# Optimization experiments

Hardware: AMD Instinct MI355X
Metric: run time of the kernel (lower is better)

The kernel has to match this reference:

```python
import jax, jax.numpy as jnp
import numpy as np

D_MODEL = 1024
D_INTERNAL = 64
SEQ = 2048
BATCH = 4


def setup_inputs() -> dict:
    key = jax.random.key(0)
    ks = jax.random.split(key, 9)
    s = 1.0 / np.sqrt(D_MODEL)
    return {
        "query": jax.random.normal(ks[0], (SEQ, BATCH, D_MODEL), jnp.float32),
        "key": jax.random.normal(ks[1], (SEQ, BATCH, D_MODEL), jnp.float32),
        "value": jax.random.normal(ks[2], (SEQ, BATCH, D_MODEL), jnp.float32),
        "Wq": jax.random.normal(ks[3], (D_MODEL, D_INTERNAL), jnp.float32) * s,
        "bq": jnp.zeros((D_INTERNAL,), jnp.float32),
        "Wk": jax.random.normal(ks[4], (D_MODEL, D_INTERNAL), jnp.float32) * s,
        "bk": jnp.zeros((D_INTERNAL,), jnp.float32),
        "Wv": jax.random.normal(ks[5], (D_MODEL, D_MODEL), jnp.float32) * s,
        "bv": jnp.zeros((D_MODEL,), jnp.float32),
    }


def reference(query, key, value, Wq, bq, Wk, bk, Wv, bv):
    # inputs: (S, B, D); project then move batch first -> (B, S, *)
    q = (query @ Wq + bq).transpose(1, 0, 2)          # (B, S, d_int)
    k = (key @ Wk + bk).transpose(1, 0, 2)            # (B, S, d_int)
    v = (value @ Wv + bv).transpose(1, 0, 2)          # (B, S, D)
    scores = jnp.einsum("bqd,bkd->bqk", q, k) / jnp.sqrt(jnp.float32(D_INTERNAL))
    probs = jax.nn.softmax(scores, axis=-1)           # row softmax over keys
    # extra renormalization over the QUERY axis (dim=1), as in the source
    probs = probs / (1e-9 + probs.sum(axis=1, keepdims=True))
    aten = jnp.einsum("bqk,bkd->bqd", probs, v).transpose(1, 0, 2)  # (S, B, D)
    return aten, probs
```

## Files before the change

### kernel.cpp

```cpp
#include <hip/hip_runtime.h>
#include <math.h>

#define SEQ 2048
#define BATCH 4
#define DM 1024
#define DI 64

typedef __attribute__((ext_vector_type(8))) short bf16x8;
typedef __attribute__((ext_vector_type(4))) float f32x4;

__device__ __forceinline__ unsigned short f2bf(float f) {
  unsigned u = __float_as_uint(f);
  unsigned r = (u + 0x7fff + ((u >> 16) & 1)) >> 16;
  return (unsigned short)r;
}

__device__ __forceinline__ float bf2f(unsigned short u) {
  return __uint_as_float((unsigned)u << 16);
}

__device__ __forceinline__ void gload_lds16(const void* g, void* l) {
  __builtin_amdgcn_global_load_lds(
      (const __attribute__((address_space(1))) unsigned int*)g,
      (__attribute__((address_space(3))) unsigned int*)l, 16, 0, 0);
}


__global__ __launch_bounds__(256) void trans_kernel(
    const float* __restrict__ Wq, const float* __restrict__ Wk,
    const float* __restrict__ Wv,
    unsigned short* __restrict__ WqkT, unsigned short* __restrict__ WvT,
    float* __restrict__ colsum) {
  __shared__ unsigned short t[64][65];
  int lx = threadIdx.x & 63, ly = threadIdx.x >> 6;
  if (blockIdx.y < 16) {
    int bx = blockIdx.x * 64, by = blockIdx.y * 64;
#pragma unroll
    for (int i = 0; i < 64; i += 4)
      t[ly + i][lx] = f2bf(Wv[(size_t)(bx + ly + i) * DM + by + lx]);
    __syncthreads();
#pragma unroll
    for (int i = 0; i < 64; i += 4)
      WvT[(size_t)(by + ly + i) * DM + bx + lx] = t[lx][ly + i];
  } else if (blockIdx.y < 18) {
    int which = blockIdx.y - 16;
    const float* W = which ? Wk : Wq;
    unsigned short* WT = WqkT + (size_t)which * DI * DM;
    int bx = blockIdx.x * 64;
#pragma unroll
    for (int i = 0; i < 64; i += 4)
      t[ly + i][lx] = f2bf(W[(size_t)(bx + ly + i) * DI + lx]);
    __syncthreads();
#pragma unroll
    for (int i = 0; i < 64; i += 4)
      WT[(size_t)(ly + i) * DM + bx + lx] = t[lx][ly + i];
  } else {
    int idx = blockIdx.x * 256 + threadIdx.x;
    colsum[idx] = 0.f;
    colsum[idx + 4096] = 0.f;
  }
}

__global__ __launch_bounds__(256) void qkproj_mfma(
    const float* __restrict__ query, const float* __restrict__ key,
    const unsigned short* __restrict__ WqkT,
    const float* __restrict__ bq, const float* __restrict__ bk,
    unsigned short* __restrict__ qbf, unsigned short* __restrict__ kbf) {
  __shared__ __align__(16) unsigned short As[32 * 32];
  __shared__ __align__(16) unsigned short Bs[64 * 32];
  int which = blockIdx.y;
  const float* A = (which ? key : query) + (size_t)blockIdx.x * 32 * DM;
  const unsigned short* Bt = WqkT + (size_t)which * DI * DM;
  const float* bias = which ? bk : bq;
  unsigned short* outp = which ? kbf : qbf;

  const int tid = threadIdx.x;
  const int lane = tid & 63, wave = tid >> 6;
  const int lrow = lane & 15, quad = lane >> 4;
  const int wr = (wave >> 1) * 16;
  const int wc = (wave & 1) * 32;
  const int sw = (quad ^ ((lrow >> 1) & 3)) * 8;
  f32x4 acc[2] = {};

  const int am = tid >> 3, asub = tid & 7;
  const int akc = asub * 4;
  const int asl = am * 32 + (((asub >> 1) ^ ((am >> 1) & 3)) * 8) + (asub & 1) * 4;
  const int bn = tid >> 2;
  const int bkc = (((tid & 3) ^ ((bn >> 1) & 3)) * 8);

  for (int k0 = 0; k0 < DM; k0 += 32) {
    __syncthreads();
    gload_lds16(Bt + (size_t)bn * DM + k0 + bkc, Bs + wave * 512);
    float4 a = *(const float4*)(A + (size_t)am * DM + k0 + akc);
    ushort4 h;
    h.x = f2bf(a.x); h.y = f2bf(a.y); h.z = f2bf(a.z); h.w = f2bf(a.w);
    *(ushort4*)&As[asl] = h;
    __syncthreads();
    bf16x8 af = *(const bf16x8*)&As[(wr + lrow) * 32 + sw];
    bf16x8 b0 = *(const bf16x8*)&Bs[(wc + lrow) * 32 + sw];
    bf16x8 b1 = *(const bf16x8*)&Bs[(wc + 16 + lrow) * 32 + sw];
    acc[0] = __builtin_amdgcn_mfma_f32_16x16x32_bf16(af, b0, acc[0], 0, 0, 0);
    acc[1] = __builtin_amdgcn_mfma_f32_16x16x32_bf16(af, b1, acc[1], 0, 0, 0);
  }
  int sbase = blockIdx.x * 8 + (wr >> 2) + quad;
#pragma unroll
  for (int ni = 0; ni < 2; ++ni) {
    int n = wc + ni * 16 + lrow;
    float bb = bias[n];
#pragma unroll
    for (int reg = 0; reg < 4; ++reg)
      outp[((size_t)reg * SEQ + sbase) * DI + n] = f2bf(acc[ni][reg] + bb);
  }
}

__global__ __launch_bounds__(256) void vcast_kernel(
    const float* __restrict__ value, unsigned short* __restrict__ vbf) {
  size_t i = ((size_t)blockIdx.x * 256 + threadIdx.x) * 8;
  float4 a = *(const float4*)(value + i);
  float4 b = *(const float4*)(value + i + 4);
  bf16x8 h;
  h[0] = (short)f2bf(a.x); h[1] = (short)f2bf(a.y);
  h[2] = (short)f2bf(a.z); h[3] = (short)f2bf(a.w);
  h[4] = (short)f2bf(b.x); h[5] = (short)f2bf(b.y);
  h[6] = (short)f2bf(b.z); h[7] = (short)f2bf(b.w);
  *(bf16x8*)(vbf + i) = h;
}

__device__ __forceinline__ void mfma_core_bb_12864(
    const unsigned short* __restrict__ At, int lda,
    const unsigned short* __restrict__ Bt, int ldb,
    int K, f32x4 (&acc)[4][2],
    unsigned short* As, unsigned short* Bs) {
  const int tid  = threadIdx.x;
  const int lane = tid & 63;
  const int wave = tid >> 6;
  const int wr   = (wave >> 1) * 64;
  const int wc   = (wave & 1) * 32;
  const int lrow = lane & 15;
  const int quad = lane >> 4;
  const int sw   = (quad ^ ((lrow >> 1) & 3)) * 8;
  const int bn   = tid >> 2;
  const int bkc  = ((tid & 3) ^ ((bn >> 1) & 3)) * 8;

  for (int k0 = 0; k0 < K; k0 += 32) {
    __syncthreads();
#pragma unroll
    for (int it = 0; it < 2; ++it) {
      int c = it * 256 + tid;
      int m = c >> 2, kc = ((c & 3) ^ ((m >> 1) & 3)) * 8;
      gload_lds16(At + (size_t)m * lda + k0 + kc,
                  As + (size_t)(it * 256 + wave * 64) * 8);
    }
    gload_lds16(Bt + (size_t)bn * ldb + k0 + bkc, Bs + wave * 512);
    __syncthreads();
    bf16x8 af[4], bfr[2];
#pragma unroll
    for (int mi = 0; mi < 4; ++mi)
      af[mi] = *(const bf16x8*)&As[(wr + mi * 16 + lrow) * 32 + sw];
#pragma unroll
    for (int ni = 0; ni < 2; ++ni)
      bfr[ni] = *(const bf16x8*)&Bs[(wc + ni * 16 + lrow) * 32 + sw];
#pragma unroll
    for (int mi = 0; mi < 4; ++mi)
#pragma unroll
      for (int ni = 0; ni < 2; ++ni)
        acc[mi][ni] = __builtin_amdgcn_mfma_f32_16x16x32_bf16(
            af[mi], bfr[ni], acc[mi][ni], 0, 0, 0);
  }
}

__global__ __launch_bounds__(256) void vproj_mfma(
    const unsigned short* __restrict__ vbf, const unsigned short* __restrict__ WvT,
    const float* __restrict__ bv, const float* __restrict__ invcol,
    unsigned short* __restrict__ vT) {
  __shared__ __align__(16) unsigned short As[128 * 32];
  __shared__ __align__(16) unsigned short Bs[64 * 32];
  __shared__ __align__(16) unsigned short ep[64 * 4 * 32];
  __shared__ float icl[128];
  f32x4 acc[4][2] = {};
  int m0 = blockIdx.x * 128, n0 = blockIdx.y * 64;
  int s0 = m0 >> 2;
  if (threadIdx.x < 128)
    icl[threadIdx.x] = invcol[(size_t)(threadIdx.x >> 5) * SEQ + s0 + (threadIdx.x & 31)];
  mfma_core_bb_12864(vbf + (size_t)m0 * DM, DM, WvT + (size_t)n0 * DM, DM, DM,
                     acc, As, Bs);
  const int tid = threadIdx.x;
  const int lane = tid & 63, wave = tid >> 6;
  const int wr = (wave >> 1) * 64, wc = (wave & 1) * 32;
  const int lrow = lane & 15, quad = lane >> 4;
#pragma unroll
  for (int mi = 0; mi < 4; ++mi) {
    int ss = (wr >> 2) + mi * 4 + quad;
#pragma unroll
    for (int ni = 0; ni < 2; ++ni) {
      int nn = wc + ni * 16 + lrow;
      float bias = bv[n0 + nn];
      int swz = (nn & 3) << 3;
#pragma unroll
      for (int reg = 0; reg < 4; ++reg)
        ep[nn * 128 + reg * 32 + (ss ^ swz)] =
            f2bf((acc[mi][ni][reg] + bias) * icl[reg * 32 + ss]);
    }
  }
  __syncthreads();
#pragma unroll
  for (int t8 = 0; t8 < 4; ++t8) {
    int c = t8 * 256 + tid;
    int ss8 = (c & 3) * 8, b = (c >> 2) & 3, nn = c >> 4;
    uint4 vv = *(const uint4*)&ep[nn * 128 + b * 32 + (ss8 ^ ((nn & 3) << 3))];
    *(uint4*)&vT[((size_t)(b * DM + n0 + nn)) * SEQ + s0 + ss8] = vv;
  }
}

__global__ __launch_bounds__(256) void scores_rowpanel(
    const unsigned short* __restrict__ qbf, const unsigned short* __restrict__ kbf,
    unsigned short* __restrict__ ebf, float* __restrict__ invrs,
    float* __restrict__ colsum) {
  __shared__ __align__(16) unsigned short Qs[16 * 64];
  __shared__ __align__(16) unsigned short Ks[128 * 64];
  __shared__ float red[4][16];
  __shared__ float irl[16];
  int bid = blockIdx.x;
  int x = bid & 7, j = bid >> 3;
  int b = x >> 1;
  int q0 = (j * 2 + (x & 1)) * 16;

  const int tid = threadIdx.x;
  const int lane = tid & 63, wave = tid >> 6;
  const int lrow = lane & 15, quad = lane >> 4;
  const int wc = wave * 32;
  const int sw = (quad ^ ((lrow >> 1) & 3)) * 8;
  const unsigned short* Q = qbf + ((size_t)b * SEQ + q0) * DI;
  const unsigned short* Kp = kbf + (size_t)b * SEQ * DI;
  unsigned short* C = ebf + (size_t)b * SEQ * SEQ;

  if (tid < 128) {
    int m = tid >> 3, kk = (tid >> 2) & 1, jj = tid & 3;
    gload_lds16(Q + (size_t)m * DI + kk * 32 + ((jj ^ ((m >> 1) & 3)) * 8),
                Qs + (size_t)(tid & ~63) * 8);
  }

  float rsum[4] = {0.f, 0.f, 0.f, 0.f};
  for (int kt = 0; kt < 16; ++kt) {
    int k0 = kt * 128;
    __syncthreads();
#pragma unroll
    for (int it = 0; it < 4; ++it) {
      int c = it * 256 + tid;
      int n = c >> 3, kk = (c >> 2) & 1, jj = c & 3;
      gload_lds16(Kp + (size_t)(k0 + n) * DI + kk * 32 + ((jj ^ ((n >> 1) & 3)) * 8),
                  Ks + (size_t)(it * 256 + wave * 64) * 8);
    }
    __syncthreads();
    bf16x8 af[2], bfr[2][2];
#pragma unroll
    for (int kk = 0; kk < 2; ++kk) {
      af[kk] = *(const bf16x8*)&Qs[lrow * 64 + kk * 32 + sw];
#pragma unroll
      for (int ni = 0; ni < 2; ++ni)
        bfr[ni][kk] = *(const bf16x8*)&Ks[(wc + ni * 16 + lrow) * 64 + kk * 32 + sw];
    }
    f32x4 acc[2] = {};
#pragma unroll
    for (int ni = 0; ni < 2; ++ni) {
      acc[ni] = __builtin_amdgcn_mfma_f32_16x16x32_bf16(af[0], bfr[ni][0], acc[ni], 0, 0, 0);
      acc[ni] = __builtin_amdgcn_mfma_f32_16x16x32_bf16(af[1], bfr[ni][1], acc[ni], 0, 0, 0);
    }
#pragma unroll
    for (int ni = 0; ni < 2; ++ni) {
      int n = k0 + wc + ni * 16 + lrow;
#pragma unroll
      for (int reg = 0; reg < 4; ++reg) {
        float e = __expf(acc[ni][reg] * 0.125f);
        C[(size_t)(q0 + quad * 4 + reg) * SEQ + n] = f2bf(e);
        rsum[reg] += e;
      }
    }
  }
  __threadfence_block();
#pragma unroll
  for (int reg = 0; reg < 4; ++reg) {
    rsum[reg] += __shfl_xor(rsum[reg], 1);
    rsum[reg] += __shfl_xor(rsum[reg], 2);
    rsum[reg] += __shfl_xor(rsum[reg], 4);
    rsum[reg] += __shfl_xor(rsum[reg], 8);
  }
  if (lrow == 0) {
#pragma unroll
    for (int reg = 0; reg < 4; ++reg) red[wave][quad * 4 + reg] = rsum[reg];
  }
  __syncthreads();
  if (tid < 16) {
    float t = red[0][tid] + red[1][tid] + red[2][tid] + red[3][tid];
    float inv = 1.0f / t;
    invrs[(size_t)b * SEQ + q0 + tid] = inv;
    irl[tid] = inv;
  }
  __syncthreads();
  int k8 = tid * 8;
  float cs[8] = {0.f, 0.f, 0.f, 0.f, 0.f, 0.f, 0.f, 0.f};
#pragma unroll 4
  for (int i = 0; i < 16; ++i) {
    const unsigned short* row = C + (size_t)(q0 + i) * SEQ + k8;
    ushort4 h0 = *(const ushort4*)(row);
    ushort4 h1 = *(const ushort4*)(row + 4);
    float ir = irl[i];
    cs[0] += bf2f(h0.x) * ir; cs[1] += bf2f(h0.y) * ir;
    cs[2] += bf2f(h0.z) * ir; cs[3] += bf2f(h0.w) * ir;
    cs[4] += bf2f(h1.x) * ir; cs[5] += bf2f(h1.y) * ir;
    cs[6] += bf2f(h1.z) * ir; cs[7] += bf2f(h1.w) * ir;
  }
#pragma unroll
  for (int jj = 0; jj < 8; ++jj)
    atomicAdd(&colsum[b * SEQ + k8 + jj], cs[jj]);
}

__global__ void recip_kernel(const float* __restrict__ in,
                             float* __restrict__ outp, float eps, int n) {
  int i = blockIdx.x * blockDim.x + threadIdx.x;
  if (i < n) outp[i] = 1.0f / (eps + in[i]);
}

__global__ __launch_bounds__(256) void probsout_kernel(
    const unsigned short* __restrict__ ebf, const float* __restrict__ invrs,
    const float* __restrict__ invcol, float* __restrict__ probs) {
  size_t f = ((size_t)blockIdx.x * 256 + threadIdx.x) * 4;
  int b = (int)(f >> 22);
  int q = (int)((f >> 11) & 2047);
  int k = (int)(f & 2047);
  ushort4 h = *(const ushort4*)(ebf + f);
  float ir = invrs[b * SEQ + q];
  float4 c = *(const float4*)(invcol + b * SEQ + k);
  float4 p;
  p.x = bf2f(h.x) * ir * c.x;
  p.y = bf2f(h.y) * ir * c.y;
  p.z = bf2f(h.z) * ir * c.z;
  p.w = bf2f(h.w) * ir * c.w;
  *(float4*)(probs + f) = p;
}

__global__ __launch_bounds__(256) void aten_mfma(
    const unsigned short* __restrict__ ebf, const unsigned short* __restrict__ vT,
    const float* __restrict__ invrs, float* __restrict__ out) {
  __shared__ __align__(16) unsigned short As[128 * 64];
  __shared__ __align__(16) unsigned short Bs[128 * 64];
  __shared__ float irs[128];
  int bid = blockIdx.x;
  int wg = (bid & 7) * 64 + (bid >> 3);
  int mb = wg & 15, nb = (wg >> 4) & 7, b = wg >> 7;
  int m0 = mb * 128, n0 = nb * 128;
  if (threadIdx.x < 128)
    irs[threadIdx.x] = invrs[(size_t)b * SEQ + m0 + threadIdx.x];
  const unsigned short* At = ebf + ((size_t)b * SEQ + m0) * SEQ;
  const unsigned short* Bt = vT + ((size_t)b * DM + n0) * SEQ;

  const int tid = threadIdx.x;
  const int lane = tid & 63, wave = tid >> 6;
  const int wr = (wave >> 1) * 64, wc = (wave & 1) * 64;
  const int lrow = lane & 15, quad = lane >> 4;
  const int sw = (quad ^ ((lrow >> 1) & 3)) * 8;

  f32x4 acc[4][4] = {};
  for (int k0 = 0; k0 < SEQ; k0 += 64) {
    __syncthreads();
#pragma unroll
    for (int it = 0; it < 4; ++it) {
      int c = it * 256 + tid;
      int m = c >> 3, kk = (c >> 2) & 1, jj = c & 3;
      gload_lds16(At + (size_t)m * SEQ + k0 + kk * 32 + ((jj ^ ((m >> 1) & 3)) * 8),
                  As + (size_t)(it * 256 + wave * 64) * 8);
    }
#pragma unroll
    for (int it = 0; it < 4; ++it) {
      int c = it * 256 + tid;
      int n = c >> 3, kk = (c >> 2) & 1, jj = c & 3;
      gload_lds16(Bt + (size_t)n * SEQ + k0 + kk * 32 + ((jj ^ ((n >> 1) & 3)) * 8),
                  Bs + (size_t)(it * 256 + wave * 64) * 8);
    }
    __syncthreads();
    bf16x8 bfr[4][2];
#pragma unroll
    for (int ni = 0; ni < 4; ++ni)
#pragma unroll
      for (int kk = 0; kk < 2; ++kk)
        bfr[ni][kk] = *(const bf16x8*)&Bs[(wc + ni * 16 + lrow) * 64 + kk * 32 + sw];
#pragma unroll
    for (int mi = 0; mi < 4; ++mi) {
      bf16x8 a0 = *(const bf16x8*)&As[(wr + mi * 16 + lrow) * 64 + sw];
      bf16x8 a1 = *(const bf16x8*)&As[(wr + mi * 16 + lrow) * 64 + 32 + sw];
#pragma unroll
      for (int ni = 0; ni < 4; ++ni) {
        acc[mi][ni] = __builtin_amdgcn_mfma_f32_16x16x32_bf16(a0, bfr[ni][0], acc[mi][ni], 0, 0, 0);
        acc[mi][ni] = __builtin_amdgcn_mfma_f32_16x16x32_bf16(a1, bfr[ni][1], acc[mi][ni], 0, 0, 0);
      }
    }
  }
#pragma unroll
  for (int mi = 0; mi < 4; ++mi) {
    int rb = wr + mi * 16 + quad * 4;
    int qr = m0 + rb;
#pragma unroll
    for (int ni = 0; ni < 4; ++ni) {
      int n = n0 + wc + ni * 16 + lrow;
#pragma unroll
      for (int reg = 0; reg < 4; ++reg)
        out[(size_t)(qr + reg) * (BATCH * DM) + b * DM + n] =
            acc[mi][ni][reg] * irs[rb + reg];
    }
  }
}

extern "C" void kernel_launch(void* const* d_in, const int* in_sizes, int n_in,
                              void* d_out, int out_size, void* d_ws, size_t ws_size,
                              hipStream_t stream) {
  const float* query = (const float*)d_in[0];
  const float* key   = (const float*)d_in[1];
  const float* value = (const float*)d_in[2];
  const float* Wq    = (const float*)d_in[3];
  const float* bq    = (const float*)d_in[4];
  const float* Wk    = (const float*)d_in[5];
  const float* bk    = (const float*)d_in[6];
  const float* Wv    = (const float*)d_in[7];
  const float* bv    = (const float*)d_in[8];

  float* out   = (float*)d_out;
  float* probs = out + (size_t)SEQ * BATCH * DM;

  unsigned short* WvT  = (unsigned short*)d_ws;
  unsigned short* WqkT = WvT  + (size_t)DM * DM;
  unsigned short* qbf  = WqkT + (size_t)2 * DI * DM;
  unsigned short* kbf  = qbf  + (size_t)BATCH * SEQ * DI;
  unsigned short* vT   = kbf  + (size_t)BATCH * SEQ * DI;
  unsigned short* ebf  = vT   + (size_t)BATCH * DM * SEQ;
  unsigned short* vbf  = ebf  + (size_t)BATCH * SEQ * SEQ;
  float* colsum = (float*)(vbf + (size_t)BATCH * SEQ * DM);
  float* invrs  = colsum + (size_t)BATCH * SEQ;
  float* invcol = invrs  + (size_t)BATCH * SEQ;

  trans_kernel<<<dim3(16, 19), 256, 0, stream>>>(Wq, Wk, Wv, WqkT, WvT, colsum);
  qkproj_mfma<<<dim3(SEQ * BATCH / 32, 2), 256, 0, stream>>>(
      query, key, WqkT, bq, bk, qbf, kbf);
  vcast_kernel<<<(SEQ * BATCH * DM / 8) / 256, 256, 0, stream>>>(value, vbf);
  scores_rowpanel<<<dim3(512), 256, 0, stream>>>(qbf, kbf, ebf, invrs, colsum);
  recip_kernel<<<(BATCH * SEQ + 255) / 256, 256, 0, stream>>>(
      colsum, invcol, 1e-9f, BATCH * SEQ);
  vproj_mfma<<<dim3(SEQ * BATCH / 128, DM / 64), 256, 0, stream>>>(
      vbf, WvT, bv, invcol, vT);
  aten_mfma<<<dim3(512), 256, 0, stream>>>(ebf, vT, invrs, out);
  probsout_kernel<<<(BATCH * SEQ * SEQ / 4) / 256, 256, 0, stream>>>(
      ebf, invrs, invcol, probs);
}
```

Measured before the change: 334.2 us.

## Merge independent kernels into shared launches and inline column reciprocal

New measurement: 378.5 us. 1.13x slower.

```diff
diff --git a/kernel.cpp b/kernel.cpp
--- a/kernel.cpp
+++ b/kernel.cpp
@@ -61,20 +61,34 @@
   }
 }
 
-__global__ __launch_bounds__(256) void qkproj_mfma(
+__global__ __launch_bounds__(256) void qkv_mix(
     const float* __restrict__ query, const float* __restrict__ key,
     const unsigned short* __restrict__ WqkT,
     const float* __restrict__ bq, const float* __restrict__ bk,
-    unsigned short* __restrict__ qbf, unsigned short* __restrict__ kbf) {
+    unsigned short* __restrict__ qbf, unsigned short* __restrict__ kbf,
+    const float* __restrict__ value, unsigned short* __restrict__ vbf) {
   __shared__ __align__(16) unsigned short As[32 * 32];
   __shared__ __align__(16) unsigned short Bs[64 * 32];
-  int which = blockIdx.y;
-  const float* A = (which ? key : query) + (size_t)blockIdx.x * 32 * DM;
+  int id = blockIdx.x;
+  const int tid = threadIdx.x;
+  if (id >= 512) {
+    size_t i = ((size_t)(id - 512) * 256 + tid) * 8;
+    float4 a = *(const float4*)(value + i);
+    float4 b = *(const float4*)(value + i + 4);
+    bf16x8 h;
+    h[0] = (short)f2bf(a.x); h[1] = (short)f2bf(a.y);
+    h[2] = (short)f2bf(a.z); h[3] = (short)f2bf(a.w);
+    h[4] = (short)f2bf(b.x); h[5] = (short)f2bf(b.y);
+    h[6] = (short)f2bf(b.z); h[7] = (short)f2bf(b.w);
+    *(bf16x8*)(vbf + i) = h;
+    return;
+  }
+  int bx = id & 255, which = id >> 8;
+  const float* A = (which ? key : query) + (size_t)bx * 32 * DM;
   const unsigned short* Bt = WqkT + (size_t)which * DI * DM;
   const float* bias = which ? bk : bq;
   unsigned short* outp = which ? kbf : qbf;
 
-  const int tid = threadIdx.x;
   const int lane = tid & 63, wave = tid >> 6;
   const int lrow = lane & 15, quad = lane >> 4;
   const int wr = (wave >> 1) * 16;
@@ -102,7 +116,7 @@
     acc[0] = __builtin_amdgcn_mfma_f32_16x16x32_bf16(af, b0, acc[0], 0, 0, 0);
     acc[1] = __builtin_amdgcn_mfma_f32_16x16x32_bf16(af, b1, acc[1], 0, 0, 0);
   }
-  int sbase = blockIdx.x * 8 + (wr >> 2) + quad;
+  int sbase = bx * 8 + (wr >> 2) + quad;
 #pragma unroll
   for (int ni = 0; ni < 2; ++ni) {
     int n = wc + ni * 16 + lrow;
@@ -111,19 +125,6 @@
     for (int reg = 0; reg < 4; ++reg)
       outp[((size_t)reg * SEQ + sbase) * DI + n] = f2bf(acc[ni][reg] + bb);
   }
-}
-
-__global__ __launch_bounds__(256) void vcast_kernel(
-    const float* __restrict__ value, unsigned short* __restrict__ vbf) {
-  size_t i = ((size_t)blockIdx.x * 256 + threadIdx.x) * 8;
-  float4 a = *(const float4*)(value + i);
-  float4 b = *(const float4*)(value + i + 4);
-  bf16x8 h;
-  h[0] = (short)f2bf(a.x); h[1] = (short)f2bf(a.y);
-  h[2] = (short)f2bf(a.z); h[3] = (short)f2bf(a.w);
-  h[4] = (short)f2bf(b.x); h[5] = (short)f2bf(b.y);
-  h[6] = (short)f2bf(b.z); h[7] = (short)f2bf(b.w);
-  *(bf16x8*)(vbf + i) = h;
 }
 
 __device__ __forceinline__ void mfma_core_bb_12864(
@@ -171,7 +172,7 @@
 
 __global__ __launch_bounds__(256) void vproj_mfma(
     const unsigned short* __restrict__ vbf, const unsigned short* __restrict__ WvT,
-    const float* __restrict__ bv, const float* __restrict__ invcol,
+    const float* __restrict__ bv, const float* __restrict__ colsum,
     unsigned short* __restrict__ vT) {
   __shared__ __align__(16) unsigned short As[128 * 32];
   __shared__ __align__(16) unsigned short Bs[64 * 32];
@@ -181,7 +182,8 @@
   int m0 = blockIdx.x * 128, n0 = blockIdx.y * 64;
   int s0 = m0 >> 2;
   if (threadIdx.x < 128)
-    icl[threadIdx.x] = invcol[(size_t)(threadIdx.x >> 5) * SEQ + s0 + (threadIdx.x & 31)];
+    icl[threadIdx.x] =
+        1.0f / (1e-9f + colsum[(size_t)(threadIdx.x >> 5) * SEQ + s0 + (threadIdx.x & 31)]);
   mfma_core_bb_12864(vbf + (size_t)m0 * DM, DM, WvT + (size_t)n0 * DM, DM, DM,
                      acc, As, Bs);
   const int tid = threadIdx.x;
@@ -315,46 +317,43 @@
     atomicAdd(&colsum[b * SEQ + k8 + jj], cs[jj]);
 }
 
-__global__ void recip_kernel(const float* __restrict__ in,
-                             float* __restrict__ outp, float eps, int n) {
-  int i = blockIdx.x * blockDim.x + threadIdx.x;
-  if (i < n) outp[i] = 1.0f / (eps + in[i]);
-}
-
-__global__ __launch_bounds__(256) void probsout_kernel(
-    const unsigned short* __restrict__ ebf, const float* __restrict__ invrs,
-    const float* __restrict__ invcol, float* __restrict__ probs) {
-  size_t f = ((size_t)blockIdx.x * 256 + threadIdx.x) * 4;
-  int b = (int)(f >> 22);
-  int q = (int)((f >> 11) & 2047);
-  int k = (int)(f & 2047);
-  ushort4 h = *(const ushort4*)(ebf + f);
-  float ir = invrs[b * SEQ + q];
-  float4 c = *(const float4*)(invcol + b * SEQ + k);
-  float4 p;
-  p.x = bf2f(h.x) * ir * c.x;
-  p.y = bf2f(h.y) * ir * c.y;
-  p.z = bf2f(h.z) * ir * c.z;
-  p.w = bf2f(h.w) * ir * c.w;
-  *(float4*)(probs + f) = p;
-}
-
-__global__ __launch_bounds__(256) void aten_mfma(
+__global__ __launch_bounds__(256) void aten_probs(
     const unsigned short* __restrict__ ebf, const unsigned short* __restrict__ vT,
-    const float* __restrict__ invrs, float* __restrict__ out) {
+    const float* __restrict__ invrs, const float* __restrict__ colsum,
+    float* __restrict__ out, float* __restrict__ probs) {
   __shared__ __align__(16) unsigned short As[128 * 64];
   __shared__ __align__(16) unsigned short Bs[128 * 64];
   __shared__ float irs[128];
-  int bid = blockIdx.x;
-  int wg = (bid & 7) * 64 + (bid >> 3);
+  int id = blockIdx.x;
+  const int tid = threadIdx.x;
+  if (id >= 512) {
+    size_t base = ((size_t)(id - 512) * 4096 + tid);
+#pragma unroll 4
+    for (int t = 0; t < 16; ++t) {
+      size_t f = (base + (size_t)t * 256) * 4;
+      int b = (int)(f >> 22);
+      int q = (int)((f >> 11) & 2047);
+      int k = (int)(f & 2047);
+      ushort4 h = *(const ushort4*)(ebf + f);
+      float ir = invrs[b * SEQ + q];
+      float4 c = *(const float4*)(colsum + b * SEQ + k);
+      float4 p;
+      p.x = bf2f(h.x) * ir * (1.0f / (1e-9f + c.x));
+      p.y = bf2f(h.y) * ir * (1.0f / (1e-9f + c.y));
+      p.z = bf2f(h.z) * ir * (1.0f / (1e-9f + c.z));
+      p.w = bf2f(h.w) * ir * (1.0f / (1e-9f + c.w));
+      *(float4*)(probs + f) = p;
+    }
+    return;
+  }
+  int wg = (id & 7) * 64 + (id >> 3);
   int mb = wg & 15, nb = (wg >> 4) & 7, b = wg >> 7;
   int m0 = mb * 128, n0 = nb * 128;
-  if (threadIdx.x < 128)
-    irs[threadIdx.x] = invrs[(size_t)b * SEQ + m0 + threadIdx.x];
+  if (tid < 128)
+    irs[tid] = invrs[(size_t)b * SEQ + m0 + tid];
   const unsigned short* At = ebf + ((size_t)b * SEQ + m0) * SEQ;
   const unsigned short* Bt = vT + ((size_t)b * DM + n0) * SEQ;
 
-  const int tid = threadIdx.x;
   const int lane = tid & 63, wave = tid >> 6;
   const int wr = (wave >> 1) * 64, wc = (wave & 1) * 64;
   const int lrow = lane & 15, quad = lane >> 4;
@@ -435,18 +434,13 @@
   unsigned short* vbf  = ebf  + (size_t)BATCH * SEQ * SEQ;
   float* colsum = (float*)(vbf + (size_t)BATCH * SEQ * DM);
   float* invrs  = colsum + (size_t)BATCH * SEQ;
-  float* invcol = invrs  + (size_t)BATCH * SEQ;
 
   trans_kernel<<<dim3(16, 19), 256, 0, stream>>>(Wq, Wk, Wv, WqkT, WvT, colsum);
-  qkproj_mfma<<<dim3(SEQ * BATCH / 32, 2), 256, 0, stream>>>(
-      query, key, WqkT, bq, bk, qbf, kbf);
-  vcast_kernel<<<(SEQ * BATCH * DM / 8) / 256, 256, 0, stream>>>(value, vbf);
+  qkv_mix<<<dim3(512 + SEQ * BATCH * DM / 8 / 256), 256, 0, stream>>>(
+      query, key, WqkT, bq, bk, qbf, kbf, value, vbf);
   scores_rowpanel<<<dim3(512), 256, 0, stream>>>(qbf, kbf, ebf, invrs, colsum);
-  recip_kernel<<<(BATCH * SEQ + 255) / 256, 256, 0, stream>>>(
-      colsum, invcol, 1e-9f, BATCH * SEQ);
   vproj_mfma<<<dim3(SEQ * BATCH / 128, DM / 64), 256, 0, stream>>>(
-      vbf, WvT, bv, invcol, vT);
-  aten_mfma<<<dim3(512), 256, 0, stream>>>(ebf, vT, invrs, out);
-  probsout_kernel<<<(BATCH * SEQ * SEQ / 4) / 256, 256, 0, stream>>>(
-      ebf, invrs, invcol, probs);
-}
+      vbf, WvT, bv, colsum, vT);
+  aten_probs<<<dim3(512 + 1024), 256, 0, stream>>>(
+      ebf, vT, invrs, colsum, out, probs);
+}
```

## Split column-sum into its own kernel, fold reciprocal into consumers, change LDS swizzle

Applied to the files above, without the earlier changes.

Result: faster. 316.8 us (-5.2%).

```diff
diff --git a/kernel.cpp b/kernel.cpp
--- a/kernel.cpp
+++ b/kernel.cpp
@@ -171,7 +171,7 @@
 
 __global__ __launch_bounds__(256) void vproj_mfma(
     const unsigned short* __restrict__ vbf, const unsigned short* __restrict__ WvT,
-    const float* __restrict__ bv, const float* __restrict__ invcol,
+    const float* __restrict__ bv, const float* __restrict__ colsum,
     unsigned short* __restrict__ vT) {
   __shared__ __align__(16) unsigned short As[128 * 32];
   __shared__ __align__(16) unsigned short Bs[64 * 32];
@@ -181,7 +181,8 @@
   int m0 = blockIdx.x * 128, n0 = blockIdx.y * 64;
   int s0 = m0 >> 2;
   if (threadIdx.x < 128)
-    icl[threadIdx.x] = invcol[(size_t)(threadIdx.x >> 5) * SEQ + s0 + (threadIdx.x & 31)];
+    icl[threadIdx.x] =
+        1.0f / (1e-9f + colsum[(size_t)(threadIdx.x >> 5) * SEQ + s0 + (threadIdx.x & 31)]);
   mfma_core_bb_12864(vbf + (size_t)m0 * DM, DM, WvT + (size_t)n0 * DM, DM, DM,
                      acc, As, Bs);
   const int tid = threadIdx.x;
@@ -214,12 +215,10 @@
 
 __global__ __launch_bounds__(256) void scores_rowpanel(
     const unsigned short* __restrict__ qbf, const unsigned short* __restrict__ kbf,
-    unsigned short* __restrict__ ebf, float* __restrict__ invrs,
-    float* __restrict__ colsum) {
+    unsigned short* __restrict__ ebf, float* __restrict__ invrs) {
   __shared__ __align__(16) unsigned short Qs[16 * 64];
   __shared__ __align__(16) unsigned short Ks[128 * 64];
   __shared__ float red[4][16];
-  __shared__ float irl[16];
   int bid = blockIdx.x;
   int x = bid & 7, j = bid >> 3;
   int b = x >> 1;
@@ -229,14 +228,16 @@
   const int lane = tid & 63, wave = tid >> 6;
   const int lrow = lane & 15, quad = lane >> 4;
   const int wc = wave * 32;
-  const int sw = (quad ^ ((lrow >> 1) & 3)) * 8;
+  const int r7 = lrow & 7;
+  const int c0 = (quad ^ r7) * 8;
+  const int c1 = ((quad + 4) ^ r7) * 8;
   const unsigned short* Q = qbf + ((size_t)b * SEQ + q0) * DI;
   const unsigned short* Kp = kbf + (size_t)b * SEQ * DI;
   unsigned short* C = ebf + (size_t)b * SEQ * SEQ;
 
   if (tid < 128) {
-    int m = tid >> 3, kk = (tid >> 2) & 1, jj = tid & 3;
-    gload_lds16(Q + (size_t)m * DI + kk * 32 + ((jj ^ ((m >> 1) & 3)) * 8),
+    int m = tid >> 3, pos = tid & 7;
+    gload_lds16(Q + (size_t)m * DI + ((pos ^ (m & 7)) * 8),
                 Qs + (size_t)(tid & ~63) * 8);
   }
 
@@ -247,18 +248,19 @@
 #pragma unroll
     for (int it = 0; it < 4; ++it) {
       int c = it * 256 + tid;
-      int n = c >> 3, kk = (c >> 2) & 1, jj = c & 3;
-      gload_lds16(Kp + (size_t)(k0 + n) * DI + kk * 32 + ((jj ^ ((n >> 1) & 3)) * 8),
+      int n = c >> 3, pos = c & 7;
+      gload_lds16(Kp + (size_t)(k0 + n) * DI + ((pos ^ (n & 7)) * 8),
                   Ks + (size_t)(it * 256 + wave * 64) * 8);
     }
     __syncthreads();
     bf16x8 af[2], bfr[2][2];
-#pragma unroll
-    for (int kk = 0; kk < 2; ++kk) {
-      af[kk] = *(const bf16x8*)&Qs[lrow * 64 + kk * 32 + sw];
-#pragma unroll
-      for (int ni = 0; ni < 2; ++ni)
-        bfr[ni][kk] = *(const bf16x8*)&Ks[(wc + ni * 16 + lrow) * 64 + kk * 32 + sw];
+    af[0] = *(const bf16x8*)&Qs[lrow * 64 + c0];
+    af[1] = *(const bf16x8*)&Qs[lrow * 64 + c1];
+#pragma unroll
+    for (int ni = 0; ni < 2; ++ni) {
+      int rr = (wc + ni * 16 + lrow) * 64;
+      bfr[ni][0] = *(const bf16x8*)&Ks[rr + c0];
+      bfr[ni][1] = *(const bf16x8*)&Ks[rr + c1];
     }
     f32x4 acc[2] = {};
 #pragma unroll
@@ -277,7 +279,6 @@
       }
     }
   }
-  __threadfence_block();
 #pragma unroll
   for (int reg = 0; reg < 4; ++reg) {
     rsum[reg] += __shfl_xor(rsum[reg], 1);
@@ -292,50 +293,39 @@
   __syncthreads();
   if (tid < 16) {
     float t = red[0][tid] + red[1][tid] + red[2][tid] + red[3][tid];
-    float inv = 1.0f / t;
-    invrs[(size_t)b * SEQ + q0 + tid] = inv;
-    irl[tid] = inv;
-  }
-  __syncthreads();
-  int k8 = tid * 8;
-  float cs[8] = {0.f, 0.f, 0.f, 0.f, 0.f, 0.f, 0.f, 0.f};
+    invrs[(size_t)b * SEQ + q0 + tid] = 1.0f / t;
+  }
+}
+
+__global__ __launch_bounds__(256) void colsum_kernel(
+    const unsigned short* __restrict__ ebf, const float* __restrict__ invrs,
+    float* __restrict__ colsum) {
+  int b = blockIdx.z;
+  int k = blockIdx.x * 256 + threadIdx.x;
+  int q0 = blockIdx.y * 128;
+  const unsigned short* p = ebf + (size_t)b * SEQ * SEQ + (size_t)q0 * SEQ + k;
+  const float* ir = invrs + (size_t)b * SEQ + q0;
+  float sum = 0.f;
 #pragma unroll 4
-  for (int i = 0; i < 16; ++i) {
-    const unsigned short* row = C + (size_t)(q0 + i) * SEQ + k8;
-    ushort4 h0 = *(const ushort4*)(row);
-    ushort4 h1 = *(const ushort4*)(row + 4);
-    float ir = irl[i];
-    cs[0] += bf2f(h0.x) * ir; cs[1] += bf2f(h0.y) * ir;
-    cs[2] += bf2f(h0.z) * ir; cs[3] += bf2f(h0.w) * ir;
-    cs[4] += bf2f(h1.x) * ir; cs[5] += bf2f(h1.y) * ir;
-    cs[6] += bf2f(h1.z) * ir; cs[7] += bf2f(h1.w) * ir;
-  }
-#pragma unroll
-  for (int jj = 0; jj < 8; ++jj)
-    atomicAdd(&colsum[b * SEQ + k8 + jj], cs[jj]);
-}
-
-__global__ void recip_kernel(const float* __restrict__ in,
-                             float* __restrict__ outp, float eps, int n) {
-  int i = blockIdx.x * blockDim.x + threadIdx.x;
-  if (i < n) outp[i] = 1.0f / (eps + in[i]);
+  for (int i = 0; i < 128; ++i) sum += bf2f(p[(size_t)i * SEQ]) * ir[i];
+  atomicAdd(&colsum[b * SEQ + k], sum);
 }
 
 __global__ __launch_bounds__(256) void probsout_kernel(
     const unsigned short* __restrict__ ebf, const float* __restrict__ invrs,
-    const float* __restrict__ invcol, float* __restrict__ probs) {
+    const float* __restrict__ colsum, float* __restrict__ probs) {
   size_t f = ((size_t)blockIdx.x * 256 + threadIdx.x) * 4;
   int b = (int)(f >> 22);
   int q = (int)((f >> 11) & 2047);
   int k = (int)(f & 2047);
   ushort4 h = *(const ushort4*)(ebf + f);
   float ir = invrs[b * SEQ + q];
-  float4 c = *(const float4*)(invcol + b * SEQ + k);
+  float4 c = *(const float4*)(colsum + b * SEQ + k);
   float4 p;
-  p.x = bf2f(h.x) * ir * c.x;
-  p.y = bf2f(h.y) * ir * c.y;
-  p.z = bf2f(h.z) * ir * c.z;
-  p.w = bf2f(h.w) * ir * c.w;
+  p.x = bf2f(h.x) * ir * (1.0f / (1e-9f + c.x));
+  p.y = bf2f(h.y) * ir * (1.0f / (1e-9f + c.y));
+  p.z = bf2f(h.z) * ir * (1.0f / (1e-9f + c.z));
+  p.w = bf2f(h.w) * ir * (1.0f / (1e-9f + c.w));
   *(float4*)(probs + f) = p;
 }
 
@@ -358,7 +348,9 @@
   const int lane = tid & 63, wave = tid >> 6;
   const int wr = (wave >> 1) * 64, wc = (wave & 1) * 64;
   const int lrow = lane & 15, quad = lane >> 4;
-  const int sw = (quad ^ ((lrow >> 1) & 3)) * 8;
+  const int r7 = lrow & 7;
+  const int c0 = (quad ^ r7) * 8;
+  const int c1 = ((quad + 4) ^ r7) * 8;
 
   f32x4 acc[4][4] = {};
   for (int k0 = 0; k0 < SEQ; k0 += 64) {
@@ -366,28 +358,30 @@
 #pragma unroll
     for (int it = 0; it < 4; ++it) {
       int c = it * 256 + tid;
-      int m = c >> 3, kk = (c >> 2) & 1, jj = c & 3;
-      gload_lds16(At + (size_t)m * SEQ + k0 + kk * 32 + ((jj ^ ((m >> 1) & 3)) * 8),
+      int m = c >> 3, pos = c & 7;
+      gload_lds16(At + (size_t)m * SEQ + k0 + ((pos ^ (m & 7)) * 8),
                   As + (size_t)(it * 256 + wave * 64) * 8);
     }
 #pragma unroll
     for (int it = 0; it < 4; ++it) {
       int c = it * 256 + tid;
-      int n = c >> 3, kk = (c >> 2) & 1, jj = c & 3;
-      gload_lds16(Bt + (size_t)n * SEQ + k0 + kk * 32 + ((jj ^ ((n >> 1) & 3)) * 8),
+      int n = c >> 3, pos = c & 7;
+      gload_lds16(Bt + (size_t)n * SEQ + k0 + ((pos ^ (n & 7)) * 8),
                   Bs + (size_t)(it * 256 + wave * 64) * 8);
     }
     __syncthreads();
     bf16x8 bfr[4][2];
 #pragma unroll
-    for (int ni = 0; ni < 4; ++ni)
-#pragma unroll
-      for (int kk = 0; kk < 2; ++kk)
-        bfr[ni][kk] = *(const bf16x8*)&Bs[(wc + ni * 16 + lrow) * 64 + kk * 32 + sw];
+    for (int ni = 0; ni < 4; ++ni) {
+      int rr = (wc + ni * 16 + lrow) * 64;
+      bfr[ni][0] = *(const bf16x8*)&Bs[rr + c0];
+      bfr[ni][1] = *(const bf16x8*)&Bs[rr + c1];
+    }
 #pragma unroll
     for (int mi = 0; mi < 4; ++mi) {
-      bf16x8 a0 = *(const bf16x8*)&As[(wr + mi * 16 + lrow) * 64 + sw];
-      bf16x8 a1 = *(const bf16x8*)&As[(wr + mi * 16 + lrow) * 64 + 32 + sw];
+      int rr = (wr + mi * 16 + lrow) * 64;
+      bf16x8 a0 = *(const bf16x8*)&As[rr + c0];
+      bf16x8 a1 = *(const bf16x8*)&As[rr + c1];
 #pragma unroll
       for (int ni = 0; ni < 4; ++ni) {
         acc[mi][ni] = __builtin_amdgcn_mfma_f32_16x16x32_bf16(a0, bfr[ni][0], acc[mi][ni], 0, 0, 0);
@@ -435,18 +429,17 @@
   unsigned short* vbf  = ebf  + (size_t)BATCH * SEQ * SEQ;
   float* colsum = (float*)(vbf + (size_t)BATCH * SEQ * DM);
   float* invrs  = colsum + (size_t)BATCH * SEQ;
-  float* invcol = invrs  + (size_t)BATCH * SEQ;
 
   trans_kernel<<<dim3(16, 19), 256, 0, stream>>>(Wq, Wk, Wv, WqkT, WvT, colsum);
   qkproj_mfma<<<dim3(SEQ * BATCH / 32, 2), 256, 0, stream>>>(
       query, key, WqkT, bq, bk, qbf, kbf);
   vcast_kernel<<<(SEQ * BATCH * DM / 8) / 256, 256, 0, stream>>>(value, vbf);
-  scores_rowpanel<<<dim3(512), 256, 0, stream>>>(qbf, kbf, ebf, invrs, colsum);
-  recip_kernel<<<(BATCH * SEQ + 255) / 256, 256, 0, stream>>>(
-      colsum, invcol, 1e-9f, BATCH * SEQ);
+  scores_rowpanel<<<dim3(512), 256, 0, stream>>>(qbf, kbf, ebf, invrs);
+  colsum_kernel<<<dim3(SEQ / 256, SEQ / 128, BATCH), 256, 0, stream>>>(
+      ebf, invrs, colsum);
   vproj_mfma<<<dim3(SEQ * BATCH / 128, DM / 64), 256, 0, stream>>>(
-      vbf, WvT, bv, invcol, vT);
+      vbf, WvT, bv, colsum, vT);
   aten_mfma<<<dim3(512), 256, 0, stream>>>(ebf, vT, invrs, out);
   probsout_kernel<<<(BATCH * SEQ * SEQ / 4) / 256, 256, 0, stream>>>(
-      ebf, invrs, invcol, probs);
-}
+      ebf, invrs, colsum, probs);
+}
```
